# Optimization experiments

Measured on AMD Instinct MI355X. Metric: run time of the kernel, lower is better.

## Reference

```python
import jax, jax.numpy as jnp
import numpy as np

DIM = 512
NUM_HEADS = 8
HEAD_DIM = DIM // NUM_HEADS
SCALE = HEAD_DIM ** -0.5


def setup_inputs() -> dict:
    key = jax.random.key(0)
    ks = jax.random.split(key, 6)
    B, N = 2, 4096
    x = jax.random.normal(ks[0], (B, N, DIM), dtype=jnp.float32)
    # xavier_uniform for qkv [3*dim, dim] and proj [dim, dim] (torch Linear weight layout [out,in])
    lim_qkv = float(np.sqrt(6.0 / (3 * DIM + DIM)))
    w_qkv = jax.random.uniform(ks[1], (3 * DIM, DIM), minval=-lim_qkv, maxval=lim_qkv, dtype=jnp.float32)
    lim_p = float(np.sqrt(6.0 / (DIM + DIM)))
    w_proj = jax.random.uniform(ks[2], (DIM, DIM), minval=-lim_p, maxval=lim_p, dtype=jnp.float32)
    b_proj = jnp.zeros((DIM,), dtype=jnp.float32)
    ln_gamma = jnp.ones((DIM,), dtype=jnp.float32)
    ln_beta = jnp.zeros((DIM,), dtype=jnp.float32)
    return {"x": x, "w_qkv": w_qkv, "w_proj": w_proj, "b_proj": b_proj,
            "ln_gamma": ln_gamma, "ln_beta": ln_beta}


def _attention(x, w_qkv, w_proj, b_proj, ln_gamma, ln_beta):
    B, N, C = x.shape
    qkv = jnp.einsum('bnc,dc->bnd', x, w_qkv)              # [B,N,3C]
    qkv = qkv.reshape(B, N, 3, NUM_HEADS, HEAD_DIM)
    qkv = jnp.transpose(qkv, (2, 0, 3, 1, 4))              # [3,B,H,N,Dh]
    q, k, v = qkv[0], qkv[1], qkv[2]
    attn = jnp.einsum('bhnd,bhmd->bhnm', q, k) * SCALE     # [B,H,N,N]
    attn = jax.nn.softmax(attn, axis=-1)
    # dropout is identity in eval mode
    out = jnp.einsum('bhnm,bhmd->bhnd', attn, v)           # [B,H,N,Dh]
    out = jnp.transpose(out, (0, 2, 1, 3)).reshape(B, N, C)
    out = jnp.einsum('bnc,dc->bnd', out, w_proj) + b_proj
    y = x + out
    mean = jnp.mean(y, axis=-1, keepdims=True)
    var = jnp.var(y, axis=-1, keepdims=True)
    return (y - mean) / jnp.sqrt(var + 1e-5) * ln_gamma + ln_beta


def reference(x, w_qkv, w_proj, b_proj, ln_gamma, ln_beta):
    return _attention(x, w_qkv, w_proj, b_proj, ln_gamma, ln_beta)
```

## Files before the change

kernel.cpp:

```cpp
#include <hip/hip_runtime.h>
#include <hip/hip_bf16.h>

#define SEQ    4096
#define CDIM   512
#define NHEADS 8
#define HDIM   64
#define QSCALE 0.18033688f

typedef __attribute__((ext_vector_type(4))) float f32x4;
typedef __attribute__((ext_vector_type(8))) short bf16x8;

__device__ __forceinline__ int swz(int row, int col) {
    int b = (row << 7) + (col << 1);
    b ^= (row & 7) << 4;
    return b >> 1;
}

__device__ __forceinline__ short f2bf(float f) {
    union { __hip_bfloat16 h; short s; } u;
    u.h = __float2bfloat16(f);
    return u.s;
}

__device__ __forceinline__ void gl16(const void* g, void* l) {
    __builtin_amdgcn_global_load_lds(
        (const __attribute__((address_space(1))) unsigned int*)g,
        (__attribute__((address_space(3))) unsigned int*)l,
        16, 0, 0);
}

__global__ __launch_bounds__(256) void cvt3_k(
    const float* __restrict__ a0, short* __restrict__ o0, int c0,
    const float* __restrict__ a1, short* __restrict__ o1, int c1,
    const float* __restrict__ a2, short* __restrict__ o2, int c2)
{
    const int total = c0 + c1 + c2;
    int i = blockIdx.x * 256 + threadIdx.x;
    const int stride = gridDim.x * 256;
    for (; i < total; i += stride) {
        const float* a; short* o; int j;
        if (i < c0)           { a = a0; o = o0; j = i; }
        else if (i < c0 + c1) { a = a1; o = o1; j = i - c0; }
        else                  { a = a2; o = o2; j = i - c0 - c1; }
        float4 v = ((const float4*)a)[j];
        short4 r;
        r.x = f2bf(v.x); r.y = f2bf(v.y); r.z = f2bf(v.z); r.w = f2bf(v.w);
        ((short4*)o)[j] = r;
    }
}

__global__ __launch_bounds__(256) void qkv_gemm_k(
    const short* __restrict__ xb, const short* __restrict__ wb,
    short* __restrict__ qb, short* __restrict__ kb, short* __restrict__ vtb)
{
    __shared__ alignas(16) short As[2][128 * 64];
    __shared__ alignas(16) short Bs[2][128 * 64];
    const int tid  = threadIdx.x;
    const int lane = tid & 63;
    const int l15  = lane & 15;
    const int lg   = lane >> 4;
    const int wv   = tid >> 6;
    const int wy   = wv >> 1, wx = wv & 1;
    const int m0 = blockIdx.x * 128;
    const int n0 = blockIdx.y * 128;

    const f32x4 fzero = {0.f, 0.f, 0.f, 0.f};
    f32x4 acc[4][4];
    #pragma unroll
    for (int i = 0; i < 4; ++i)
        #pragma unroll
        for (int j = 0; j < 4; ++j)
            acc[i][j] = fzero;

    const int row0 = wv * 8 + (lane >> 3);
    const int cb   = ((lane & 7) ^ (lane >> 3)) << 4;
    const char* agp = (const char*)xb + (size_t)(m0 + row0) * 1024 + cb;
    const char* bgp = (const char*)wb + (size_t)(n0 + row0) * 1024 + cb;
    char* al0 = (char*)&As[0][0] + wv * 1024;
    char* al1 = (char*)&As[1][0] + wv * 1024;
    char* bl0 = (char*)&Bs[0][0] + wv * 1024;
    char* bl1 = (char*)&Bs[1][0] + wv * 1024;

    #define QSTAGE(al, bl, kofs) do {                                  \
        _Pragma("unroll")                                              \
        for (int i_ = 0; i_ < 4; ++i_) {                               \
            gl16(agp + (kofs) + i_ * 32768, (al) + i_ * 4096);         \
            gl16(bgp + (kofs) + i_ * 32768, (bl) + i_ * 4096);         \
        } } while (0)

    QSTAGE(al0, bl0, 0);

    int cur = 0;
    for (int k0 = 0; k0 < CDIM; k0 += 64) {
        asm volatile("s_waitcnt vmcnt(0)" ::: "memory");
        __syncthreads();
        if (k0 + 64 < CDIM) {
            if (cur == 0) QSTAGE(al1, bl1, (k0 + 64) * 2);
            else          QSTAGE(al0, bl0, (k0 + 64) * 2);
        }
        const short* Ac = cur ? &As[1][0] : &As[0][0];
        const short* Bc = cur ? &Bs[1][0] : &Bs[0][0];

        #pragma unroll
        for (int ks = 0; ks < 2; ++ks) {
            bf16x8 afr[4], bfr[4];
            #pragma unroll
            for (int i = 0; i < 4; ++i) {
                afr[i] = *(const bf16x8*)(&Ac[swz(wy * 64 + i * 16 + l15, ks * 32 + lg * 8)]);
                bfr[i] = *(const bf16x8*)(&Bc[swz(wx * 64 + i * 16 + l15, ks * 32 + lg * 8)]);
            }
            #pragma unroll
            for (int i = 0; i < 4; ++i)
                #pragma unroll
                for (int j = 0; j < 4; ++j)
                    acc[i][j] = __builtin_amdgcn_mfma_f32_16x16x32_bf16(afr[i], bfr[j], acc[i][j], 0, 0, 0);
        }
        cur ^= 1;
    }
    #undef QSTAGE

    #pragma unroll
    for (int j = 0; j < 4; ++j) {
        const int d = n0 + wx * 64 + j * 16 + l15;
        const int s = d >> 9;
        const int h = (d >> 6) & 7;
        const int e = d & 63;
        #pragma unroll
        for (int i = 0; i < 4; ++i) {
            #pragma unroll
            for (int r = 0; r < 4; ++r) {
                const int m  = m0 + wy * 64 + i * 16 + lg * 4 + r;
                const int bb = m >> 12;
                const int n  = m & (SEQ - 1);
                const int bh = bb * NHEADS + h;
                const float v = acc[i][j][r];
                if (s == 0) {
                    qb[(((size_t)bh * SEQ + n) << 6) + e] = f2bf(v * QSCALE);
                } else if (s == 1) {
                    kb[(((size_t)bh * SEQ + n) << 6) + e] = f2bf(v);
                } else {
                    const int c  = n & 31;
                    const int cp = (c & 3) | ((c & 0x0C) << 1) | ((c & 0x10) >> 2);
                    vtb[((size_t)bh << 18) + ((size_t)(n >> 5) << 11) + (e << 5) + cp] = f2bf(v);
                }
            }
        }
    }
}

__global__ __launch_bounds__(512) void attn_k(
    const short* __restrict__ qb, const short* __restrict__ kb, const short* __restrict__ vtb,
    short* __restrict__ ob)
{
    __shared__ alignas(16) char smem[65536];
    const int tid  = threadIdx.x;
    const int lane = tid & 63;
    const int l15  = lane & 15;
    const int lg   = lane >> 4;
    const int wv   = (tid >> 6) & 3;
    const int wg   = tid >> 8;
    const int lin  = blockIdx.x;
    const int bh   = lin & 15;
    const int q0   = (lin >> 4) << 7;
    const int b    = bh >> 3, h = bh & 7;
    const size_t base = (size_t)bh * SEQ * HDIM;

    bf16x8 qf[2][2];
    #pragma unroll
    for (int qi = 0; qi < 2; ++qi) {
        const short* qp = qb + base + (size_t)(q0 + wv * 32 + qi * 16 + l15) * HDIM + lg * 8;
        qf[qi][0] = *(const bf16x8*)(qp);
        qf[qi][1] = *(const bf16x8*)(qp + 32);
    }

    const f32x4 fzero = {0.f, 0.f, 0.f, 0.f};
    f32x4 acc[2][4];
    f32x4 lacc[2];
    #pragma unroll
    for (int qi = 0; qi < 2; ++qi) {
        lacc[qi] = fzero;
        #pragma unroll
        for (int di = 0; di < 4; ++di) acc[qi][di] = fzero;
    }

    bf16x8 ones;
    #pragma unroll
    for (int e = 0; e < 8; ++e) ones[e] = (short)0x3F80;

    const int t0  = wv * 64 + lane;
    const int cbs = ((t0 & 7) ^ ((t0 >> 3) & 7)) << 4;
    const int ghb = wg * 262144;
    const char* kgp = (const char*)(kb + base) + ghb + (((t0 >> 3) << 7) + cbs);
    const char* vgp = (const char*)(vtb + ((size_t)bh << 18)) + ghb + (((t0 >> 3) << 7) + cbs);
    char* const gb = smem + wg * 32768;
    const short* Kb0 = (const short*)(gb);
    const short* Kb1 = (const short*)(gb + 4096);
    const short* Kb2 = (const short*)(gb + 8192);
    const short* Kb3 = (const short*)(gb + 12288);
    const short* Vb0 = (const short*)(gb + 16384);
    const short* Vb1 = (const short*)(gb + 20480);
    const short* Vb2 = (const short*)(gb + 24576);
    const short* Vb3 = (const short*)(gb + 28672);
    char* Ks0 = gb +     0 + wv * 1024;
    char* Ks1 = gb +  4096 + wv * 1024;
    char* Ks2 = gb +  8192 + wv * 1024;
    char* Ks3 = gb + 12288 + wv * 1024;
    char* Vs0 = gb + 16384 + wv * 1024;
    char* Vs1 = gb + 20480 + wv * 1024;
    char* Vs2 = gb + 24576 + wv * 1024;
    char* Vs3 = gb + 28672 + wv * 1024;

    #define MFMA16(a_, b_, c_) __builtin_amdgcn_mfma_f32_16x16x32_bf16(a_, b_, c_, 0, 0, 0)

    #define STAGE2(T_, KS, VS) do {                    \
        gl16(kgp + (T_) * 4096, (KS));                 \
        gl16(vgp + (T_) * 4096, (VS));                 \
    } while (0)

    #define COMPUTE(KR, VR) do {                                               \
        f32x4 s00 = fzero, s01 = fzero, s10 = fzero, s11 = fzero;              \
        __builtin_amdgcn_s_setprio(1);                                         \
        {                                                                      \
            bf16x8 kf_;                                                        \
            kf_ = *(const bf16x8*)(&(KR)[swz(l15, lg * 8)]);                   \
            s00 = MFMA16(kf_, qf[0][0], s00);                                  \
            s10 = MFMA16(kf_, qf[1][0], s10);                                  \
            kf_ = *(const bf16x8*)(&(KR)[swz(l15, 32 + lg * 8)]);              \
            s00 = MFMA16(kf_, qf[0][1], s00);                                  \
            s10 = MFMA16(kf_, qf[1][1], s10);                                  \
            kf_ = *(const bf16x8*)(&(KR)[swz(16 + l15, lg * 8)]);              \
            s01 = MFMA16(kf_, qf[0][0], s01);                                  \
            s11 = MFMA16(kf_, qf[1][0], s11);                                  \
            kf_ = *(const bf16x8*)(&(KR)[swz(16 + l15, 32 + lg * 8)]);         \
            s01 = MFMA16(kf_, qf[0][1], s01);                                  \
            s11 = MFMA16(kf_, qf[1][1], s11);                                  \
        }                                                                      \
        __builtin_amdgcn_s_setprio(0);                                         \
        bf16x8 pa0, pa1;                                                       \
        _Pragma("unroll")                                                      \
        for (int r_ = 0; r_ < 4; ++r_) {                                       \
            pa0[r_]     = f2bf(__builtin_amdgcn_exp2f(s00[r_]));               \
            pa0[4 + r_] = f2bf(__builtin_amdgcn_exp2f(s01[r_]));               \
            pa1[r_]     = f2bf(__builtin_amdgcn_exp2f(s10[r_]));               \
            pa1[4 + r_] = f2bf(__builtin_amdgcn_exp2f(s11[r_]));               \
        }                                                                      \
        __builtin_amdgcn_s_setprio(1);                                         \
        lacc[0] = MFMA16(pa0, ones, lacc[0]);                                  \
        lacc[1] = MFMA16(pa1, ones, lacc[1]);                                  \
        _Pragma("unroll")                                                      \
        for (int di_ = 0; di_ < 4; ++di_) {                                    \
            bf16x8 vf_ = *(const bf16x8*)(&(VR)[swz(di_ * 8 + (l15 >> 1),      \
                                                    (l15 & 1) * 32 + lg * 8)]);\
            acc[0][di_] = MFMA16(pa0, vf_, acc[0][di_]);                       \
            acc[1][di_] = MFMA16(pa1, vf_, acc[1][di_]);                       \
        }                                                                      \
        __builtin_amdgcn_s_setprio(0);                                         \
    } while (0)

    #define STEP(T_, KR, VR, KS, VS) do {                          \
        asm volatile("s_waitcnt vmcnt(4)" ::: "memory");           \
        __builtin_amdgcn_s_barrier();                              \
        asm volatile("" ::: "memory");                             \
        if ((T_) < 61) { STAGE2((T_) + 3, KS, VS); }               \
        COMPUTE(KR, VR);                                           \
    } while (0)

    STAGE2(0, Ks0, Vs0);
    STAGE2(1, Ks1, Vs1);
    STAGE2(2, Ks2, Vs2);

    for (int it = 0; it < 16; ++it) {
        const int t = it << 2;
        STEP(t + 0, Kb0, Vb0, Ks3, Vs3);
        STEP(t + 1, Kb1, Vb1, Ks0, Vs0);
        STEP(t + 2, Kb2, Vb2, Ks1, Vs1);
        STEP(t + 3, Kb3, Vb3, Ks2, Vs2);
    }
    #undef STEP
    #undef COMPUTE
    #undef STAGE2
    #undef MFMA16

    __syncthreads();
    float* xch = (float*)smem;
    const int xi = (wv * 64 + lane) * 44;
    if (wg == 1) {
        #pragma unroll
        for (int qi = 0; qi < 2; ++qi) {
            #pragma unroll
            for (int di = 0; di < 4; ++di)
                *(f32x4*)(xch + xi + qi * 16 + di * 4) = acc[qi][di];
            *(f32x4*)(xch + xi + 32 + qi * 4) = lacc[qi];
        }
    }
    __syncthreads();
    if (wg == 0) {
        #pragma unroll
        for (int qi = 0; qi < 2; ++qi) {
            #pragma unroll
            for (int di = 0; di < 4; ++di)
                acc[qi][di] += *(const f32x4*)(xch + xi + qi * 16 + di * 4);
            lacc[qi] += *(const f32x4*)(xch + xi + 32 + qi * 4);
        }
        #pragma unroll
        for (int qi = 0; qi < 2; ++qi) {
            float inv[4];
            #pragma unroll
            for (int r = 0; r < 4; ++r) inv[r] = 1.0f / lacc[qi][r];
            #pragma unroll
            for (int di = 0; di < 4; ++di) {
                const int e = di * 16 + l15;
                #pragma unroll
                for (int r = 0; r < 4; ++r) {
                    const int qn = q0 + wv * 32 + qi * 16 + lg * 4 + r;
                    ob[((size_t)(b * SEQ + qn) << 9) + h * 64 + e] = f2bf(acc[qi][di][r] * inv[r]);
                }
            }
        }
    }
}

__global__ __launch_bounds__(256) void proj_k(
    const short* __restrict__ ao, const short* __restrict__ wpb,
    const float* __restrict__ bp, const float* __restrict__ x,
    float* __restrict__ y)
{
    __shared__ alignas(16) short As[2][128 * 64];
    __shared__ alignas(16) short Bs[2][128 * 64];
    const int tid  = threadIdx.x;
    const int lane = tid & 63;
    const int l15  = lane & 15;
    const int lg   = lane >> 4;
    const int wv   = tid >> 6;
    const int wy   = wv >> 1, wx = wv & 1;
    const int m0 = blockIdx.x * 128;
    const int n0 = blockIdx.y * 128;

    const f32x4 fzero = {0.f, 0.f, 0.f, 0.f};
    f32x4 acc[4][4];
    #pragma unroll
    for (int i = 0; i < 4; ++i)
        #pragma unroll
        for (int j = 0; j < 4; ++j)
            acc[i][j] = fzero;

    const int row0 = wv * 8 + (lane >> 3);
    const int cb   = ((lane & 7) ^ (lane >> 3)) << 4;
    const char* agp = (const char*)ao  + (size_t)(m0 + row0) * 1024 + cb;
    const char* bgp = (const char*)wpb + (size_t)(n0 + row0) * 1024 + cb;
    char* al0 = (char*)&As[0][0] + wv * 1024;
    char* al1 = (char*)&As[1][0] + wv * 1024;
    char* bl0 = (char*)&Bs[0][0] + wv * 1024;
    char* bl1 = (char*)&Bs[1][0] + wv * 1024;

    #define PSTAGE(al, bl, kofs) do {                                  \
        _Pragma("unroll")                                              \
        for (int i_ = 0; i_ < 4; ++i_) {                               \
            gl16(agp + (kofs) + i_ * 32768, (al) + i_ * 4096);         \
            gl16(bgp + (kofs) + i_ * 32768, (bl) + i_ * 4096);         \
        } } while (0)

    PSTAGE(al0, bl0, 0);

    int cur = 0;
    for (int k0 = 0; k0 < CDIM; k0 += 64) {
        asm volatile("s_waitcnt vmcnt(0)" ::: "memory");
        __syncthreads();
        if (k0 + 64 < CDIM) {
            if (cur == 0) PSTAGE(al1, bl1, (k0 + 64) * 2);
            else          PSTAGE(al0, bl0, (k0 + 64) * 2);
        }
        const short* Ac = cur ? &As[1][0] : &As[0][0];
        const short* Bc = cur ? &Bs[1][0] : &Bs[0][0];

        #pragma unroll
        for (int ks = 0; ks < 2; ++ks) {
            bf16x8 afr[4], bfr[4];
            #pragma unroll
            for (int i = 0; i < 4; ++i) {
                afr[i] = *(const bf16x8*)(&Ac[swz(wy * 64 + i * 16 + l15, ks * 32 + lg * 8)]);
                bfr[i] = *(const bf16x8*)(&Bc[swz(wx * 64 + i * 16 + l15, ks * 32 + lg * 8)]);
            }
            #pragma unroll
            for (int i = 0; i < 4; ++i)
                #pragma unroll
                for (int j = 0; j < 4; ++j)
                    acc[i][j] = __builtin_amdgcn_mfma_f32_16x16x32_bf16(afr[i], bfr[j], acc[i][j], 0, 0, 0);
        }
        cur ^= 1;
    }
    #undef PSTAGE

    #pragma unroll
    for (int i = 0; i < 4; ++i) {
        #pragma unroll
        for (int j = 0; j < 4; ++j) {
            const int d = n0 + wx * 64 + j * 16 + l15;
            #pragma unroll
            for (int r = 0; r < 4; ++r) {
                const int m = m0 + wy * 64 + i * 16 + lg * 4 + r;
                const size_t idx = (size_t)m * CDIM + d;
                y[idx] = acc[i][j][r] + bp[d] + x[idx];
            }
        }
    }
}

__global__ __launch_bounds__(256) void ln_k(
    float* __restrict__ y, const float* __restrict__ gm, const float* __restrict__ bt)
{
    const int lane = threadIdx.x & 63;
    const int row  = blockIdx.x * 4 + (threadIdx.x >> 6);
    float* p = y + (size_t)row * CDIM;
    float4 a = *(const float4*)(p + lane * 4);
    float4 b = *(const float4*)(p + 256 + lane * 4);
    float s = a.x + a.y + a.z + a.w + b.x + b.y + b.z + b.w;
    float q = a.x * a.x + a.y * a.y + a.z * a.z + a.w * a.w
            + b.x * b.x + b.y * b.y + b.z * b.z + b.w * b.w;
    #pragma unroll
    for (int mm = 1; mm < 64; mm <<= 1) {
        s += __shfl_xor(s, mm, 64);
        q += __shfl_xor(q, mm, 64);
    }
    const float mean = s * (1.0f / CDIM);
    const float var  = q * (1.0f / CDIM) - mean * mean;
    const float inv  = rsqrtf(var + 1e-5f);
    float4 g0 = *(const float4*)(gm + lane * 4);
    float4 g1 = *(const float4*)(gm + 256 + lane * 4);
    float4 t0 = *(const float4*)(bt + lane * 4);
    float4 t1 = *(const float4*)(bt + 256 + lane * 4);
    float4 r0, r1;
    r0.x = (a.x - mean) * inv * g0.x + t0.x;
    r0.y = (a.y - mean) * inv * g0.y + t0.y;
    r0.z = (a.z - mean) * inv * g0.z + t0.z;
    r0.w = (a.w - mean) * inv * g0.w + t0.w;
    r1.x = (b.x - mean) * inv * g1.x + t1.x;
    r1.y = (b.y - mean) * inv * g1.y + t1.y;
    r1.z = (b.z - mean) * inv * g1.z + t1.z;
    r1.w = (b.w - mean) * inv * g1.w + t1.w;
    *(float4*)(p + lane * 4) = r0;
    *(float4*)(p + 256 + lane * 4) = r1;
}

extern "C" void kernel_launch(void* const* d_in, const int* in_sizes, int n_in,
                              void* d_out, int out_size, void* d_ws, size_t ws_size,
                              hipStream_t stream)
{
    const float* x      = (const float*)d_in[0];
    const float* w_qkv  = (const float*)d_in[1];
    const float* w_proj = (const float*)d_in[2];
    const float* b_proj = (const float*)d_in[3];
    const float* gamma  = (const float*)d_in[4];
    const float* beta   = (const float*)d_in[5];
    float* out = (float*)d_out;

    const size_t qkv_elems = (size_t)16 * SEQ * HDIM;
    short* qb    = (short*)d_ws;
    short* kb    = qb + qkv_elems;
    short* vtb   = kb + qkv_elems;
    short* ob    = vtb + qkv_elems;
    short* xb    = ob;
    short* wqkvb = ob + qkv_elems;
    short* wpb   = wqkvb + (size_t)3 * CDIM * CDIM;

    cvt3_k    <<<dim3(1024),   256, 0, stream>>>(
        x, xb, (2 * SEQ * CDIM) / 4,
        w_qkv, wqkvb, (3 * CDIM * CDIM) / 4,
        w_proj, wpb, (CDIM * CDIM) / 4);
    qkv_gemm_k<<<dim3(64, 12), 256, 0, stream>>>(xb, wqkvb, qb, kb, vtb);
    attn_k    <<<dim3(512),    512, 0, stream>>>(qb, kb, vtb, ob);
    proj_k    <<<dim3(64, 4),  256, 0, stream>>>(ob, wpb, b_proj, x, out);
    ln_k      <<<dim3(2048),   256, 0, stream>>>(out, gamma, beta);
}
```

Baseline: 111.3 us.

## Deepen GEMM pipelines to four stages and peel attention loop tail

Both the QKV and projection GEMMs move from a double-buffered 64-wide K step with full vmcnt(0) waits to a four-buffer, 32-wide K pipeline. Loads run three stages ahead and waits are partial, and the MFMA section gets a raised priority. The attention main loop is peeled so the last iterations drain with smaller vmcnt counts instead of a per-step conditional. The aim is to hide global-to-LDS latency in the GEMMs, at the cost of more barriers per K and a new swizzle layout.

```diff
diff --git a/kernel.cpp b/kernel.cpp
--- a/kernel.cpp
+++ b/kernel.cpp
@@ -14,6 +14,10 @@
     int b = (row << 7) + (col << 1);
     b ^= (row & 7) << 4;
     return b >> 1;
+}
+
+__device__ __forceinline__ int swz64(int row, int c) {
+    return ((row << 6) + (((c) ^ ((row >> 1) & 3)) << 4)) >> 1;
 }
 
 __device__ __forceinline__ short f2bf(float f) {
@@ -49,75 +53,82 @@
     }
 }
 
+
+#define GEMM_PRELUDE(APTR, BPTR)                                               \
+    __shared__ alignas(16) short As[4][128 * 32];                              \
+    __shared__ alignas(16) short Bs[4][128 * 32];                              \
+    const int tid  = threadIdx.x;                                              \
+    const int lane = tid & 63;                                                 \
+    const int l15  = lane & 15;                                                \
+    const int lg   = lane >> 4;                                                \
+    const int wv   = tid >> 6;                                                 \
+    const int wy   = wv >> 1, wx = wv & 1;                                     \
+    const int m0 = blockIdx.x * 128;                                           \
+    const int n0 = blockIdx.y * 128;                                           \
+    const f32x4 fzero = {0.f, 0.f, 0.f, 0.f};                                  \
+    f32x4 acc[4][4];                                                           \
+    _Pragma("unroll")                                                          \
+    for (int i = 0; i < 4; ++i)                                                \
+        _Pragma("unroll")                                                      \
+        for (int j = 0; j < 4; ++j)                                            \
+            acc[i][j] = fzero;                                                 \
+      \
+    const int srow = wv * 32 + (lane >> 2);                                    \
+    const int scb  = ((lane & 3) ^ ((lane >> 3) & 3)) << 4;                    \
+    const char* agp = (const char*)(APTR) + (size_t)(m0 + srow) * 1024 + scb;  \
+    const char* bgp = (const char*)(BPTR) + (size_t)(n0 + srow) * 1024 + scb;  \
+    const int ldst = wv * 2048;
+
+#define GSTAGE(T_, BUF_) do {                                                  \
+    _Pragma("unroll")                                                          \
+    for (int i_ = 0; i_ < 2; ++i_) {                                           \
+        gl16(agp + (T_) * 64 + i_ * 16384, (char*)&As[BUF_][0] + ldst + i_ * 1024); \
+        gl16(bgp + (T_) * 64 + i_ * 16384, (char*)&Bs[BUF_][0] + ldst + i_ * 1024); \
+    } } while (0)
+
+#define GCOMP(BUF_) do {                                                       \
+    bf16x8 afr[4], bfr[4];                                                     \
+    _Pragma("unroll")                                                          \
+    for (int i = 0; i < 4; ++i) {                                              \
+        afr[i] = *(const bf16x8*)(&As[BUF_][swz64(wy * 64 + i * 16 + l15, lg)]); \
+        bfr[i] = *(const bf16x8*)(&Bs[BUF_][swz64(wx * 64 + i * 16 + l15, lg)]); \
+    }                                                                          \
+    __builtin_amdgcn_s_setprio(1);                                             \
+    _Pragma("unroll")                                                          \
+    for (int i = 0; i < 4; ++i)                                                \
+        _Pragma("unroll")                                                      \
+        for (int j = 0; j < 4; ++j)                                            \
+            acc[i][j] = __builtin_amdgcn_mfma_f32_16x16x32_bf16(afr[i], bfr[j], acc[i][j], 0, 0, 0); \
+    __builtin_amdgcn_s_setprio(0);                                             \
+} while (0)
+
+#define GWAITBAR(N_) do {                                                      \
+    asm volatile("s_waitcnt vmcnt(" #N_ ")" ::: "memory");                     \
+    __builtin_amdgcn_s_barrier();                                              \
+    asm volatile("" ::: "memory");                                             \
+} while (0)
+
+#define GEMM_MAIN                                                              \
+    GSTAGE(0, 0); GSTAGE(1, 1); GSTAGE(2, 2);                                  \
+    _Pragma("unroll")                                                          \
+    for (int it = 0; it < 3; ++it) {                                           \
+        const int t = it * 4;                                                  \
+        GWAITBAR(8); GSTAGE(t + 3, 3); GCOMP(0);                               \
+        GWAITBAR(8); GSTAGE(t + 4, 0); GCOMP(1);                               \
+        GWAITBAR(8); GSTAGE(t + 5, 1); GCOMP(2);                               \
+        GWAITBAR(8); GSTAGE(t + 6, 2); GCOMP(3);                               \
+    }                                                                          \
+    GWAITBAR(8); GSTAGE(15, 3); GCOMP(0);                                      \
+    GWAITBAR(8); GCOMP(1);                                                     \
+    GWAITBAR(4); GCOMP(2);                                                     \
+    GWAITBAR(0); GCOMP(3);
+
 __global__ __launch_bounds__(256) void qkv_gemm_k(
     const short* __restrict__ xb, const short* __restrict__ wb,
     short* __restrict__ qb, short* __restrict__ kb, short* __restrict__ vtb)
 {
-    __shared__ alignas(16) short As[2][128 * 64];
-    __shared__ alignas(16) short Bs[2][128 * 64];
-    const int tid  = threadIdx.x;
-    const int lane = tid & 63;
-    const int l15  = lane & 15;
-    const int lg   = lane >> 4;
-    const int wv   = tid >> 6;
-    const int wy   = wv >> 1, wx = wv & 1;
-    const int m0 = blockIdx.x * 128;
-    const int n0 = blockIdx.y * 128;
-
-    const f32x4 fzero = {0.f, 0.f, 0.f, 0.f};
-    f32x4 acc[4][4];
-    #pragma unroll
-    for (int i = 0; i < 4; ++i)
-        #pragma unroll
-        for (int j = 0; j < 4; ++j)
-            acc[i][j] = fzero;
-
-    const int row0 = wv * 8 + (lane >> 3);
-    const int cb   = ((lane & 7) ^ (lane >> 3)) << 4;
-    const char* agp = (const char*)xb + (size_t)(m0 + row0) * 1024 + cb;
-    const char* bgp = (const char*)wb + (size_t)(n0 + row0) * 1024 + cb;
-    char* al0 = (char*)&As[0][0] + wv * 1024;
-    char* al1 = (char*)&As[1][0] + wv * 1024;
-    char* bl0 = (char*)&Bs[0][0] + wv * 1024;
-    char* bl1 = (char*)&Bs[1][0] + wv * 1024;
-
-    #define QSTAGE(al, bl, kofs) do {                                  \
-        _Pragma("unroll")                                              \
-        for (int i_ = 0; i_ < 4; ++i_) {                               \
-            gl16(agp + (kofs) + i_ * 32768, (al) + i_ * 4096);         \
-            gl16(bgp + (kofs) + i_ * 32768, (bl) + i_ * 4096);         \
-        } } while (0)
-
-    QSTAGE(al0, bl0, 0);
-
-    int cur = 0;
-    for (int k0 = 0; k0 < CDIM; k0 += 64) {
-        asm volatile("s_waitcnt vmcnt(0)" ::: "memory");
-        __syncthreads();
-        if (k0 + 64 < CDIM) {
-            if (cur == 0) QSTAGE(al1, bl1, (k0 + 64) * 2);
-            else          QSTAGE(al0, bl0, (k0 + 64) * 2);
-        }
-        const short* Ac = cur ? &As[1][0] : &As[0][0];
-        const short* Bc = cur ? &Bs[1][0] : &Bs[0][0];
-
-        #pragma unroll
-        for (int ks = 0; ks < 2; ++ks) {
-            bf16x8 afr[4], bfr[4];
-            #pragma unroll
-            for (int i = 0; i < 4; ++i) {
-                afr[i] = *(const bf16x8*)(&Ac[swz(wy * 64 + i * 16 + l15, ks * 32 + lg * 8)]);
-                bfr[i] = *(const bf16x8*)(&Bc[swz(wx * 64 + i * 16 + l15, ks * 32 + lg * 8)]);
-            }
-            #pragma unroll
-            for (int i = 0; i < 4; ++i)
-                #pragma unroll
-                for (int j = 0; j < 4; ++j)
-                    acc[i][j] = __builtin_amdgcn_mfma_f32_16x16x32_bf16(afr[i], bfr[j], acc[i][j], 0, 0, 0);
-        }
-        cur ^= 1;
-    }
-    #undef QSTAGE
+    GEMM_PRELUDE(xb, wb)
+    GEMM_MAIN
 
     #pragma unroll
     for (int j = 0; j < 4; ++j) {
@@ -143,6 +154,29 @@
                     const int cp = (c & 3) | ((c & 0x0C) << 1) | ((c & 0x10) >> 2);
                     vtb[((size_t)bh << 18) + ((size_t)(n >> 5) << 11) + (e << 5) + cp] = f2bf(v);
                 }
+            }
+        }
+    }
+}
+
+__global__ __launch_bounds__(256) void proj_k(
+    const short* __restrict__ ao, const short* __restrict__ wpb,
+    const float* __restrict__ bp, const float* __restrict__ x,
+    float* __restrict__ y)
+{
+    GEMM_PRELUDE(ao, wpb)
+    GEMM_MAIN
+
+    #pragma unroll
+    for (int i = 0; i < 4; ++i) {
+        #pragma unroll
+        for (int j = 0; j < 4; ++j) {
+            const int d = n0 + wx * 64 + j * 16 + l15;
+            #pragma unroll
+            for (int r = 0; r < 4; ++r) {
+                const int m = m0 + wy * 64 + i * 16 + lg * 4 + r;
+                const size_t idx = (size_t)m * CDIM + d;
+                y[idx] = acc[i][j][r] + bp[d] + x[idx];
             }
         }
     }
@@ -257,26 +291,28 @@
         __builtin_amdgcn_s_setprio(0);                                         \
     } while (0)
 
-    #define STEP(T_, KR, VR, KS, VS) do {                          \
-        asm volatile("s_waitcnt vmcnt(4)" ::: "memory");           \
+    #define AWAITBAR(N_) do {                                      \
+        asm volatile("s_waitcnt vmcnt(" #N_ ")" ::: "memory");     \
         __builtin_amdgcn_s_barrier();                              \
         asm volatile("" ::: "memory");                             \
-        if ((T_) < 61) { STAGE2((T_) + 3, KS, VS); }               \
-        COMPUTE(KR, VR);                                           \
     } while (0)
 
     STAGE2(0, Ks0, Vs0);
     STAGE2(1, Ks1, Vs1);
     STAGE2(2, Ks2, Vs2);
 
-    for (int it = 0; it < 16; ++it) {
+    for (int it = 0; it < 15; ++it) {
         const int t = it << 2;
-        STEP(t + 0, Kb0, Vb0, Ks3, Vs3);
-        STEP(t + 1, Kb1, Vb1, Ks0, Vs0);
-        STEP(t + 2, Kb2, Vb2, Ks1, Vs1);
-        STEP(t + 3, Kb3, Vb3, Ks2, Vs2);
-    }
-    #undef STEP
+        AWAITBAR(4); STAGE2(t + 3, Ks3, Vs3); COMPUTE(Kb0, Vb0);
+        AWAITBAR(4); STAGE2(t + 4, Ks0, Vs0); COMPUTE(Kb1, Vb1);
+        AWAITBAR(4); STAGE2(t + 5, Ks1, Vs1); COMPUTE(Kb2, Vb2);
+        AWAITBAR(4); STAGE2(t + 6, Ks2, Vs2); COMPUTE(Kb3, Vb3);
+    }
+    AWAITBAR(4); STAGE2(63, Ks3, Vs3); COMPUTE(Kb0, Vb0);
+    AWAITBAR(4); COMPUTE(Kb1, Vb1);
+    AWAITBAR(2); COMPUTE(Kb2, Vb2);
+    AWAITBAR(0); COMPUTE(Kb3, Vb3);
+    #undef AWAITBAR
     #undef COMPUTE
     #undef STAGE2
     #undef MFMA16
@@ -315,92 +351,6 @@
                     const int qn = q0 + wv * 32 + qi * 16 + lg * 4 + r;
                     ob[((size_t)(b * SEQ + qn) << 9) + h * 64 + e] = f2bf(acc[qi][di][r] * inv[r]);
                 }
-            }
-        }
-    }
-}
-
-__global__ __launch_bounds__(256) void proj_k(
-    const short* __restrict__ ao, const short* __restrict__ wpb,
-    const float* __restrict__ bp, const float* __restrict__ x,
-    float* __restrict__ y)
-{
-    __shared__ alignas(16) short As[2][128 * 64];
-    __shared__ alignas(16) short Bs[2][128 * 64];
-    const int tid  = threadIdx.x;
-    const int lane = tid & 63;
-    const int l15  = lane & 15;
-    const int lg   = lane >> 4;
-    const int wv   = tid >> 6;
-    const int wy   = wv >> 1, wx = wv & 1;
-    const int m0 = blockIdx.x * 128;
-    const int n0 = blockIdx.y * 128;
-
-    const f32x4 fzero = {0.f, 0.f, 0.f, 0.f};
-    f32x4 acc[4][4];
-    #pragma unroll
-    for (int i = 0; i < 4; ++i)
-        #pragma unroll
-        for (int j = 0; j < 4; ++j)
-            acc[i][j] = fzero;
-
-    const int row0 = wv * 8 + (lane >> 3);
-    const int cb   = ((lane & 7) ^ (lane >> 3)) << 4;
-    const char* agp = (const char*)ao  + (size_t)(m0 + row0) * 1024 + cb;
-    const char* bgp = (const char*)wpb + (size_t)(n0 + row0) * 1024 + cb;
-    char* al0 = (char*)&As[0][0] + wv * 1024;
-    char* al1 = (char*)&As[1][0] + wv * 1024;
-    char* bl0 = (char*)&Bs[0][0] + wv * 1024;
-    char* bl1 = (char*)&Bs[1][0] + wv * 1024;
-
-    #define PSTAGE(al, bl, kofs) do {                                  \
-        _Pragma("unroll")                                              \
-        for (int i_ = 0; i_ < 4; ++i_) {                               \
-            gl16(agp + (kofs) + i_ * 32768, (al) + i_ * 4096);         \
-            gl16(bgp + (kofs) + i_ * 32768, (bl) + i_ * 4096);         \
-        } } while (0)
-
-    PSTAGE(al0, bl0, 0);
-
-    int cur = 0;
-    for (int k0 = 0; k0 < CDIM; k0 += 64) {
-        asm volatile("s_waitcnt vmcnt(0)" ::: "memory");
-        __syncthreads();
-        if (k0 + 64 < CDIM) {
-            if (cur == 0) PSTAGE(al1, bl1, (k0 + 64) * 2);
-            else          PSTAGE(al0, bl0, (k0 + 64) * 2);
-        }
-        const short* Ac = cur ? &As[1][0] : &As[0][0];
-        const short* Bc = cur ? &Bs[1][0] : &Bs[0][0];
-
-        #pragma unroll
-        for (int ks = 0; ks < 2; ++ks) {
-            bf16x8 afr[4], bfr[4];
-            #pragma unroll
-            for (int i = 0; i < 4; ++i) {
-                afr[i] = *(const bf16x8*)(&Ac[swz(wy * 64 + i * 16 + l15, ks * 32 + lg * 8)]);
-                bfr[i] = *(const bf16x8*)(&Bc[swz(wx * 64 + i * 16 + l15, ks * 32 + lg * 8)]);
-            }
-            #pragma unroll
-            for (int i = 0; i < 4; ++i)
-                #pragma unroll
-                for (int j = 0; j < 4; ++j)
-                    acc[i][j] = __builtin_amdgcn_mfma_f32_16x16x32_bf16(afr[i], bfr[j], acc[i][j], 0, 0, 0);
-        }
-        cur ^= 1;
-    }
-    #undef PSTAGE
-
-    #pragma unroll
-    for (int i = 0; i < 4; ++i) {
-        #pragma unroll
-        for (int j = 0; j < 4; ++j) {
-            const int d = n0 + wx * 64 + j * 16 + l15;
-            #pragma unroll
-            for (int r = 0; r < 4; ++r) {
-                const int m = m0 + wy * 64 + i * 16 + lg * 4 + r;
-                const size_t idx = (size_t)m * CDIM + d;
-                y[idx] = acc[i][j][r] + bp[d] + x[idx];
             }
         }
     }
```

Result: slower. 121.1 us (+8.8%).
